# Kernel optimization log

Measured on AMD Instinct MI355X. Metric: run time of the kernel, lower is better.

Reference implementation:

```python
import jax, jax.numpy as jnp
import numpy as np
import math

DIM, H, Q_RANK, KV_RANK = 2048, 16, 768, 512
QK_STATIC, QK_ROT, V_DIM = 128, 64, 128
QK_TOTAL = QK_STATIC + QK_ROT
BS, SEQ = 2, 1024


def rmsnorm(x, scale, eps=1e-6):
    xf = x.astype(jnp.float32)
    return scale * (xf * jax.lax.rsqrt(jnp.mean(xf * xf, axis=-1, keepdims=True) + eps))


def half_rotate(x):
    h = x.shape[-1] // 2
    return jnp.concatenate([-x[..., h:], x[..., :h]], axis=-1)


def rope_tables(seq_len, dim):
    inv_freq = 1.0 / (10000.0 ** (jnp.arange(0, dim, 2, dtype=jnp.float32) / dim))
    freqs = jnp.arange(seq_len, dtype=jnp.float32)[:, None] * inv_freq[None, :]
    cos = jnp.concatenate([jnp.cos(freqs), jnp.cos(freqs)], axis=-1)  # (S, dim)
    sin = jnp.concatenate([jnp.sin(freqs), jnp.sin(freqs)], axis=-1)
    return cos, sin


def setup_inputs() -> dict:
    key = jax.random.key(0)
    ks = jax.random.split(key, 10)
    sc = lambda fan_in: 1.0 / math.sqrt(fan_in)
    x = jax.random.normal(ks[0], (BS, SEQ, DIM), dtype=jnp.float32)
    causal = jnp.where(jnp.tril(jnp.ones((SEQ, SEQ), dtype=bool)), 0.0, -1e9).astype(jnp.float32)
    mask = jnp.broadcast_to(causal[None], (BS, SEQ, SEQ))
    return {
        "x": x,
        "start_pos": 0,
        "mask": mask,
        "q_down_w": jax.random.normal(ks[1], (Q_RANK, DIM)) * sc(DIM),
        "q_down_b": jnp.zeros((Q_RANK,), jnp.float32),
        "q_norm_scale": jnp.ones((Q_RANK,), jnp.float32),
        "q_up_w": jax.random.normal(ks[2], (H * QK_TOTAL, Q_RANK)) * sc(Q_RANK),
        "q_up_b": jnp.zeros((H * QK_TOTAL,), jnp.float32),
        "kv_down_w": jax.random.normal(ks[3], (KV_RANK + QK_ROT, DIM)) * sc(DIM),
        "kv_down_b": jnp.zeros((KV_RANK + QK_ROT,), jnp.float32),
        "kv_norm_scale": jnp.ones((KV_RANK,), jnp.float32),
        "kv_up_w": jax.random.normal(ks[4], (H * (QK_STATIC + V_DIM), KV_RANK)) * sc(KV_RANK),
        "out_w": jax.random.normal(ks[5], (DIM, H * V_DIM)) * sc(H * V_DIM),
        "out_b": jnp.zeros((DIM,), jnp.float32),
    }


def reference(x, start_pos, mask, q_down_w, q_down_b, q_norm_scale, q_up_w, q_up_b,
              kv_down_w, kv_down_b, kv_norm_scale, kv_up_w, out_w, out_b):
    bs, seq_len, _ = x.shape
    # q path: down-proj -> RMSNorm -> up-proj
    q = rmsnorm(x @ q_down_w.T + q_down_b, q_norm_scale)
    q = (q @ q_up_w.T + q_up_b).reshape(bs, seq_len, H, QK_TOTAL)
    q_static, q_rot = q[..., :QK_STATIC], q[..., QK_STATIC:]
    # kv path: shared down-proj producing latent features + rotary key part
    kv = x @ kv_down_w.T + kv_down_b
    kv_feat, k_rot = kv[..., :KV_RANK], kv[..., KV_RANK:]
    # RoPE (original indexes positions 0..seq_len-1)
    cos, sin = rope_tables(seq_len, QK_ROT)
    q_rot = q_rot * cos[None, :, None, :] + half_rotate(q_rot) * sin[None, :, None, :]
    k_rot = k_rot * cos[None, :, :] + half_rotate(k_rot) * sin[None, :, :]  # (b, t, r)
    kv_normed = rmsnorm(kv_feat, kv_norm_scale)  # latent cache contents (b, t, c)
    # matrix absorption: fold kv_up key-weights into q
    w_k_abs = kv_up_w[: H * QK_STATIC, :].reshape(H, QK_STATIC, KV_RANK)
    w_v_abs = kv_up_w[-H * V_DIM :, :].reshape(H, V_DIM, KV_RANK)
    q_static_proj = jnp.einsum('bshd,hdc->bshc', q_static, w_k_abs)
    attn_scores = (jnp.einsum('bshc,btc->bsht', q_static_proj, kv_normed)
                   + jnp.einsum('bshr,btr->bsht', q_rot, k_rot)) / math.sqrt(QK_TOTAL)
    attn_scores = attn_scores + mask[:, :, None, :]
    attn_weights = jax.nn.softmax(attn_scores, axis=-1)
    # attend over latent features, then expand with absorbed value weights
    ctx_c = jnp.einsum('bsht,btc->bshc', attn_weights, kv_normed)
    ctx = jnp.einsum('bshc,hdc->bshd', ctx_c, w_v_abs)
    out = ctx.reshape(bs, seq_len, H * V_DIM) @ out_w.T + out_b
    return out
```

## Files before the change

kernel.cpp:

```cpp
#include <hip/hip_runtime.h>
#include <stdint.h>
#include <stddef.h>


typedef __attribute__((ext_vector_type(8))) short bf16x8;
typedef __attribute__((ext_vector_type(4))) float f32x4;

__device__ inline float b2f(unsigned short v){
    union { unsigned u; float f; } x; x.u = ((unsigned)v) << 16; return x.f;
}
__device__ inline unsigned short f2b(float f){
    union { float f; unsigned u; } x; x.f = f;
    unsigned r = x.u + 0x7fffu + ((x.u >> 16) & 1u);
    return (unsigned short)(r >> 16);
}

__device__ __forceinline__ void gl2lds16(const unsigned short* g, unsigned short* l){
    __builtin_amdgcn_global_load_lds(
        (__attribute__((address_space(1))) void*)const_cast<unsigned short*>(g),
        (__attribute__((address_space(3))) void*)l,
        16, 0, 0);
}

template<typename TC>
static __device__ __forceinline__ void gemm_body(
    unsigned short (*As)[4096], unsigned short (*Bs)[4096],
    const unsigned short* A, const unsigned short* B,
    const float* bias, TC* C,
    int N, int K, int lda, int ldb, int ldc,
    int m0, int n0, float alpha, int causal)
{
    const int tid = threadIdx.x, w = tid >> 6, lane = tid & 63;
    const int wm = w >> 1, wn = w & 1;

    const int srow = w * 32 + (lane >> 2);
    const int schunk = ((lane & 3) ^ ((lane >> 3) & 3)) * 8;
    const unsigned short* gA = A + (size_t)(m0 + srow) * lda + schunk;
    const unsigned short* gB = B + (size_t)(n0 + srow) * ldb + schunk;

    const int ktiles = K >> 5;
    auto stage = [&](int buf, int kt){
        const int k0 = kt << 5;
        gl2lds16(gA + k0,            &As[buf][w * 1024]);
        gl2lds16(gA + k0 + 16 * lda, &As[buf][w * 1024 + 512]);
        gl2lds16(gB + k0,            &Bs[buf][w * 1024]);
        gl2lds16(gB + k0 + 16 * ldb, &Bs[buf][w * 1024 + 512]);
    };
    stage(0, 0);
    if (ktiles > 1) stage(1, 1);

    f32x4 acc[4][4] = {};
    const int lm = lane & 15;
    const int kq = (((lane >> 4) ^ (lm >> 1)) & 3) * 8;

    int cur = 0;
    for (int kt = 0; kt < ktiles; ++kt){
        if (kt + 1 < ktiles) __builtin_amdgcn_s_waitcnt(0xF74);
        else                 __builtin_amdgcn_s_waitcnt(0xF70);
        __builtin_amdgcn_s_barrier();
        __asm__ volatile("" ::: "memory");
        if (kt + 2 < ktiles) stage(cur >= 1 ? cur - 1 : 2, kt + 2);
        bf16x8 af[4], bfr[4];
        #pragma unroll
        for (int i = 0; i < 4; ++i)
            af[i] = *(const bf16x8*)&As[cur][(wm * 64 + i * 16 + lm) * 32 + kq];
        #pragma unroll
        for (int j = 0; j < 4; ++j)
            bfr[j] = *(const bf16x8*)&Bs[cur][(wn * 64 + j * 16 + lm) * 32 + kq];
        #pragma unroll
        for (int i = 0; i < 4; ++i)
            #pragma unroll
            for (int j = 0; j < 4; ++j)
                acc[i][j] = __builtin_amdgcn_mfma_f32_16x16x32_bf16(af[i], bfr[j], acc[i][j], 0, 0, 0);
        __asm__ volatile("" ::: "memory");
        cur = (cur == 2) ? 0 : cur + 1;
    }

    #pragma unroll
    for (int i = 0; i < 4; ++i){
        const int m = m0 + wm * 64 + i * 16 + (lane >> 4) * 4;
        #pragma unroll
        for (int j = 0; j < 4; ++j){
            const int n = n0 + wn * 64 + j * 16 + lm;
            if (n < N){
                const float bb = bias ? bias[n] : 0.f;
                #pragma unroll
                for (int r = 0; r < 4; ++r){
                    float v = acc[i][j][r] * alpha + bb;
                    if ((causal & 1) && n > m + r) v = -1e9f;
                    if constexpr (sizeof(TC) == 2)
                        C[(size_t)(m + r) * ldc + n] = (TC)f2b(v);
                    else
                        C[(size_t)(m + r) * ldc + n] = (TC)v;
                }
            }
        }
    }
}

template<typename TC>
__global__ __launch_bounds__(256) void mfma_gemm_bt(
    const unsigned short* __restrict__ A, const unsigned short* __restrict__ B,
    const float* __restrict__ bias, TC* __restrict__ C,
    int M, int N, int K, int lda, int ldb, int ldc,
    int zdiv, long sA_hi, long sA_lo, long sB_hi, long sB_lo, long sC_hi, long sC_lo,
    float alpha, int causal)
{
    int z, bm, bn;
    if (causal & 4){ z = blockIdx.x; bm = blockIdx.y; bn = blockIdx.z; }
    else           { z = blockIdx.z; bm = blockIdx.y; bn = blockIdx.x; }
    int m0, n0;
    if (causal & 1){
        int i = bm;
        int mt = (int)((sqrtf(8.f * i + 1.f) - 1.f) * 0.5f);
        while ((mt + 1) * (mt + 2) / 2 <= i) ++mt;
        while (mt * (mt + 1) / 2 > i) --mt;
        n0 = (i - mt * (mt + 1) / 2) * 128;
        m0 = mt * 128;
    } else { m0 = bm * 128; n0 = bn * 128; }
    if (causal & 2) K = min(K, m0 + 128);

    __shared__ unsigned short As[3][4096];
    __shared__ unsigned short Bs[3][4096];
    const int zh = z / zdiv, zl = z % zdiv;
    A += (size_t)zh * sA_hi + (size_t)zl * sA_lo;
    B += (size_t)zh * sB_hi + (size_t)zl * sB_lo;
    C += (size_t)zh * sC_hi + (size_t)zl * sC_lo;

    gemm_body<TC>(As, Bs, A, B, bias, C, N, K, lda, ldb, ldc, m0, n0, alpha, causal);
}

__global__ __launch_bounds__(256) void mfma_gemm_vk(
    const unsigned short* __restrict__ kvuw,
    const unsigned short* __restrict__ kcat,
    unsigned short* __restrict__ vhT,
    unsigned short* __restrict__ khcat)
{
    __shared__ unsigned short As[3][4096];
    __shared__ unsigned short Bs[3][4096];
    const int p = blockIdx.x & 1, z = blockIdx.x >> 1, y = blockIdx.y;
    const int b = z >> 4, h = z & 15;
    if (p == 0){
        const unsigned short* A = kvuw + 1048576 + (size_t)h * 65536;
        const unsigned short* B = kcat + (size_t)b * 589824;
        unsigned short* C = vhT + (size_t)b * 2097152 + (size_t)h * 131072;
        gemm_body<unsigned short>(As, Bs, A, B, nullptr, C,
                                  1024, 512, 512, 576, 1024, 0, y * 128, 1.0f, 0);
    } else {
        const unsigned short* A = kcat + (size_t)b * 589824;
        const unsigned short* B = kvuw + (size_t)h * 65536;
        unsigned short* C = khcat + (size_t)b * 3145728 + (size_t)h * 196608;
        gemm_body<unsigned short>(As, Bs, A, B, nullptr, C,
                                  128, 512, 576, 512, 192, y * 128, 0, 1.0f, 0);
    }
}

__global__ __launch_bounds__(256) void flash_attn(
    const unsigned short* __restrict__ qu,
    const unsigned short* __restrict__ khcat,
    const unsigned short* __restrict__ vhT,
    unsigned short* __restrict__ ctx)
{
    const int t = blockIdx.x;
    const int r = t & 7, q = t >> 3;
    const int z = r + 8 * (q & 3);
    const int u = q >> 2;
    const int mt = (u < 8) ? (15 - 2 * u) : (2 * (u - 8));
    const int b = z >> 4, h = z & 15;
    const int m0 = mt * 64;
    const int nkt = (mt >> 1) + 1;

    __shared__ char smem[74240];
    unsigned short (*Qs)[4096] = (unsigned short (*)[4096])smem;
    unsigned short (*Ks)[8192] = (unsigned short (*)[8192])(smem + 24576);
    unsigned short* Ps = (unsigned short*)(smem + 24576);
    float* lrow = (float*)(smem + 73728);

    const unsigned short* kB = khcat + (size_t)z * 196608;
    const unsigned short* vB = vhT + (size_t)z * 131072;

    const int tid = threadIdx.x, w = tid >> 6, lane = tid & 63;
    const int wm = w >> 1, wn = w & 1;
    const int lm = lane & 15, g = lane >> 4;
    const int kq = g * 8;
    const int rs7 = lm & 7;

    if (tid < 128) lrow[tid] = 0.f;

    const int srow8 = lane >> 3;
    const int soff8 = ((lane & 7) ^ (lane >> 3)) * 8;
    const unsigned short* gQ = qu + (size_t)(b * 1024 + m0 + w * 16 + srow8) * 3072
                               + h * 192 + soff8;

    #pragma unroll
    for (int c = 0; c < 3; ++c){
        gl2lds16(gQ + c * 64,            &Qs[c][w * 1024]);
        gl2lds16(gQ + c * 64 + 8 * 3072, &Qs[c][w * 1024 + 512]);
    }

    auto stageK = [&](int buf, int kt, int c){
        const unsigned short* gK = kB + (size_t)(kt * 128 + w * 32 + srow8) * 192
                                   + c * 64 + soff8;
        gl2lds16(gK,            &Ks[buf][w * 2048]);
        gl2lds16(gK + 8 * 192,  &Ks[buf][w * 2048 + 512]);
        gl2lds16(gK + 16 * 192, &Ks[buf][w * 2048 + 1024]);
        gl2lds16(gK + 24 * 192, &Ks[buf][w * 2048 + 1536]);
    };
    stageK(2, 0, 0);

    f32x4 Oacc[2][4] = {};
    const float scl = 0.07216878364870322f;

    for (int kt = 0; kt < nkt; ++kt){
        stageK(0, kt, 1);
        stageK(1, kt, 2);
        __asm__ volatile("" ::: "memory");
        bf16x8 vfr[4][4];
        #pragma unroll
        for (int j = 0; j < 4; ++j)
            #pragma unroll
            for (int kc = 0; kc < 4; ++kc)
                vfr[j][kc] = *(const bf16x8*)(vB + (size_t)(wn * 64 + j * 16 + lm) * 1024
                                              + kt * 128 + kc * 32 + kq);
        __asm__ volatile("" ::: "memory");

        f32x4 S[2][4] = {};
        #pragma unroll
        for (int c = 0; c < 3; ++c){
            if      (c == 0) __builtin_amdgcn_s_waitcnt(0x4F78);
            else if (c == 1) __builtin_amdgcn_s_waitcnt(0x4F74);
            else             __builtin_amdgcn_s_waitcnt(0x4F70);
            __builtin_amdgcn_s_barrier();
            __asm__ volatile("" ::: "memory");
            const int bufc = (c == 0) ? 2 : (c - 1);
            bf16x8 af[2][2], bfr[4][2];
            #pragma unroll
            for (int i = 0; i < 2; ++i)
                #pragma unroll
                for (int kk = 0; kk < 2; ++kk)
                    af[i][kk] = *(const bf16x8*)&Qs[c][(wm * 32 + i * 16 + lm) * 64
                                                       + (((kk * 4 + g) ^ rs7) * 8)];
            #pragma unroll
            for (int j = 0; j < 4; ++j)
                #pragma unroll
                for (int kk = 0; kk < 2; ++kk)
                    bfr[j][kk] = *(const bf16x8*)&Ks[bufc][(wn * 64 + j * 16 + lm) * 64
                                                           + (((kk * 4 + g) ^ rs7) * 8)];
            __builtin_amdgcn_s_setprio(1);
            #pragma unroll
            for (int kk = 0; kk < 2; ++kk)
                #pragma unroll
                for (int i = 0; i < 2; ++i)
                    #pragma unroll
                    for (int j = 0; j < 4; ++j)
                        S[i][j] = __builtin_amdgcn_mfma_f32_16x16x32_bf16(af[i][kk], bfr[j][kk], S[i][j], 0, 0, 0);
            __builtin_amdgcn_s_setprio(0);
            __asm__ volatile("" ::: "memory");
        }
        __builtin_amdgcn_s_waitcnt(0xC07F);
        __builtin_amdgcn_s_barrier();
        __asm__ volatile("" ::: "memory");
        if (kt + 1 < nkt) stageK(2, kt + 1, 0);

        const bool diag = (kt == (mt >> 1));
        #pragma unroll
        for (int i = 0; i < 2; ++i){
            float rs[4] = {0.f, 0.f, 0.f, 0.f};
            #pragma unroll
            for (int j = 0; j < 4; ++j){
                const int nloc = wn * 64 + j * 16 + lm;
                #pragma unroll
                for (int r2 = 0; r2 < 4; ++r2){
                    const int mloc = wm * 32 + i * 16 + g * 4 + r2;
                    float p = __expf(S[i][j][r2] * scl);
                    if (diag && (kt * 128 + nloc) > (m0 + mloc)) p = 0.f;
                    rs[r2] += p;
                    Ps[mloc * 136 + nloc] = f2b(p);
                }
            }
            #pragma unroll
            for (int r2 = 0; r2 < 4; ++r2){
                rs[r2] += __shfl_xor(rs[r2], 1, 64);
                rs[r2] += __shfl_xor(rs[r2], 2, 64);
                rs[r2] += __shfl_xor(rs[r2], 4, 64);
                rs[r2] += __shfl_xor(rs[r2], 8, 64);
            }
            if (lm == 0){
                #pragma unroll
                for (int r2 = 0; r2 < 4; ++r2)
                    lrow[wn * 64 + wm * 32 + i * 16 + g * 4 + r2] += rs[r2];
            }
        }
        __asm__ volatile("" ::: "memory");
        __builtin_amdgcn_s_waitcnt(0xC07F);
        __builtin_amdgcn_s_barrier();
        __asm__ volatile("" ::: "memory");

        if (kt + 1 < nkt) __builtin_amdgcn_s_waitcnt(0xF74);
        else              __builtin_amdgcn_s_waitcnt(0xF70);
        #pragma unroll
        for (int kc = 0; kc < 4; ++kc){
            bf16x8 pa[2];
            #pragma unroll
            for (int i = 0; i < 2; ++i)
                pa[i] = *(const bf16x8*)&Ps[(wm * 32 + i * 16 + lm) * 136 + kc * 32 + kq];
            __builtin_amdgcn_s_setprio(1);
            #pragma unroll
            for (int i = 0; i < 2; ++i)
                #pragma unroll
                for (int j = 0; j < 4; ++j)
                    Oacc[i][j] = __builtin_amdgcn_mfma_f32_16x16x32_bf16(pa[i], vfr[j][kc], Oacc[i][j], 0, 0, 0);
            __builtin_amdgcn_s_setprio(0);
        }
        __asm__ volatile("" ::: "memory");
        __builtin_amdgcn_s_waitcnt(0xC07F);
        __builtin_amdgcn_s_barrier();
        __asm__ volatile("" ::: "memory");
    }

    unsigned short* cBase = ctx + ((size_t)(b * 1024 + m0)) * 2048 + h * 128;
    #pragma unroll
    for (int i = 0; i < 2; ++i){
        #pragma unroll
        for (int r2 = 0; r2 < 4; ++r2){
            const int row = wm * 32 + i * 16 + g * 4 + r2;
            const float inv = 1.f / (lrow[row] + lrow[64 + row]);
            #pragma unroll
            for (int j = 0; j < 4; ++j){
                const int col = wn * 64 + j * 16 + lm;
                cBase[(size_t)row * 2048 + col] = f2b(Oacc[i][j][r2] * inv);
            }
        }
    }
}

__global__ __launch_bounds__(256) void cast_all(
    const float* __restrict__ s0, unsigned short* __restrict__ d0,
    const float* __restrict__ s1, unsigned short* __restrict__ d1,
    const float* __restrict__ s2, unsigned short* __restrict__ d2,
    const float* __restrict__ s3, unsigned short* __restrict__ d3,
    const float* __restrict__ s4, unsigned short* __restrict__ d4,
    const float* __restrict__ s5, unsigned short* __restrict__ d5)
{
    long i = (long)(blockIdx.x * 256 + threadIdx.x) * 4;
    const float* s; unsigned short* d; long off;
    if      (i <  4194304L){ s = s0; d = d0; off = i; }
    else if (i <  5767168L){ s = s1; d = d1; off = i -  4194304L; }
    else if (i <  8126464L){ s = s2; d = d2; off = i -  5767168L; }
    else if (i <  9306112L){ s = s3; d = d3; off = i -  8126464L; }
    else if (i < 11403264L){ s = s4; d = d4; off = i -  9306112L; }
    else                   { s = s5; d = d5; off = i - 11403264L; }
    float4 v = *(const float4*)(s + off);
    *(ushort4*)(d + off) = make_ushort4(f2b(v.x), f2b(v.y), f2b(v.z), f2b(v.w));
}

__global__ __launch_bounds__(256) void fused_down_post(
    const unsigned short* __restrict__ p,
    const float* __restrict__ q_down_b, const float* __restrict__ kv_down_b,
    const float* __restrict__ q_norm_s, const float* __restrict__ kv_norm_s,
    unsigned short* __restrict__ qn, unsigned short* __restrict__ kcat)
{
    __shared__ float row[1344];
    __shared__ float red[4];
    const int t = blockIdx.x, tid = threadIdx.x;
    const long S = 2752512L;
    const unsigned short* b0 = p + (size_t)t * 1344;
    for (int c = tid; c < 1344; c += 256){
        float v = b2f(b0[c]) + b2f(b0[c + S]) + b2f(b0[c + 2*S]) + b2f(b0[c + 3*S]);
        v += (c < 768) ? q_down_b[c] : kv_down_b[c - 768];
        row[c] = v;
    }
    __syncthreads();
    const int lane = tid & 63, w = tid >> 6;
    float ss = 0.f;
    for (int c = tid; c < 768; c += 256){ float v = row[c]; ss += v * v; }
    #pragma unroll
    for (int o = 32; o > 0; o >>= 1) ss += __shfl_xor(ss, o, 64);
    if (lane == 0) red[w] = ss;
    __syncthreads();
    const float inv1 = rsqrtf((red[0]+red[1]+red[2]+red[3]) / 768.f + 1e-6f);
    __syncthreads();
    ss = 0.f;
    for (int c = tid; c < 512; c += 256){ float v = row[768 + c]; ss += v * v; }
    #pragma unroll
    for (int o = 32; o > 0; o >>= 1) ss += __shfl_xor(ss, o, 64);
    if (lane == 0) red[w] = ss;
    __syncthreads();
    const float inv2 = rsqrtf((red[0]+red[1]+red[2]+red[3]) / 512.f + 1e-6f);
    for (int c = tid; c < 768; c += 256)
        qn[(size_t)t * 768 + c] = f2b(q_norm_s[c] * row[c] * inv1);
    for (int c = tid; c < 512; c += 256)
        kcat[(size_t)t * 576 + c] = f2b(kv_norm_s[c] * row[768 + c] * inv2);
    if (tid < 64){
        const int d = tid, s = t & 1023;
        float x  = row[1280 + d];
        float xp = (d < 32) ? -row[1280 + d + 32] : row[1280 + d - 32];
        float ang = (float)s * powf(10000.f, -(float)(2 * (d & 31)) / 64.f);
        kcat[(size_t)t * 576 + 512 + d] = f2b(x * cosf(ang) + xp * sinf(ang));
    }
}

__global__ __launch_bounds__(256) void reduce_out(
    const unsigned short* __restrict__ p, const float* __restrict__ bias,
    float* __restrict__ out)
{
    const long S = 4194304L;
    long i = (long)(blockIdx.x * 256 + threadIdx.x) * 4;
    ushort4 a = *(const ushort4*)(p + i);
    ushort4 b = *(const ushort4*)(p + i + S);
    float4 bb = *(const float4*)(bias + (i & 2047));
    float4 r = make_float4(b2f(a.x) + b2f(b.x) + bb.x, b2f(a.y) + b2f(b.y) + bb.y,
                           b2f(a.z) + b2f(b.z) + bb.z, b2f(a.w) + b2f(b.w) + bb.w);
    *(float4*)(out + i) = r;
}

__global__ __launch_bounds__(256) void rope_q_krot(
    unsigned short* __restrict__ qu,
    const unsigned short* __restrict__ kcat,
    unsigned short* __restrict__ khcat)
{
    long idx = (long)blockIdx.x * 256 + threadIdx.x;
    if (idx < 1048576L){
        const int d   = idx & 31;
        const int h   = (idx >> 5) & 15;
        const int tok = idx >> 9;
        const int s   = tok & 1023;
        unsigned short* base = qu + (size_t)tok * 3072 + h * 192 + 128;
        float x1 = b2f(base[d]), x2 = b2f(base[d + 32]);
        float ang = (float)s * powf(10000.f, -(float)d / 32.f);
        float c = cosf(ang), sn = sinf(ang);
        base[d]      = f2b(x1 * c - x2 * sn);
        base[d + 32] = f2b(x2 * c + x1 * sn);
    } else {
        idx -= 1048576L;
        const int d   = idx & 63;
        const int h   = (idx >> 6) & 15;
        const int tok = (int)(idx >> 10);
        const int bb  = tok >> 10, s = tok & 1023;
        khcat[((size_t)(bb * 16 + h) * 1024 + s) * 192 + 128 + d] =
            kcat[(size_t)tok * 576 + 512 + d];
    }
}

extern "C" void kernel_launch(void* const* d_in, const int* in_sizes, int n_in,
                              void* d_out, int out_size, void* d_ws, size_t ws_size,
                              hipStream_t stream)
{
    const float* x         = (const float*)d_in[0];
    const float* q_down_w  = (const float*)d_in[3];
    const float* q_down_b  = (const float*)d_in[4];
    const float* q_norm_s  = (const float*)d_in[5];
    const float* q_up_w    = (const float*)d_in[6];
    const float* q_up_b    = (const float*)d_in[7];
    const float* kv_down_w = (const float*)d_in[8];
    const float* kv_down_b = (const float*)d_in[9];
    const float* kv_norm_s = (const float*)d_in[10];
    const float* kv_up_w   = (const float*)d_in[11];
    const float* out_w     = (const float*)d_in[12];
    const float* out_b     = (const float*)d_in[13];
    float* out = (float*)d_out;

    char* ws = (char*)d_ws;
    unsigned short* kvuw  = (unsigned short*)(ws + 0);
    unsigned short* outw  = (unsigned short*)(ws + 4194304);
    unsigned short* kcat  = (unsigned short*)(ws + 12582912);
    unsigned short* vhT   = (unsigned short*)(ws + 14942208);
    unsigned short* khcat = (unsigned short*)(ws + 23330816);
    unsigned short* ctx   = (unsigned short*)(ws + 35913728);
    unsigned short* qu    = (unsigned short*)(ws + 44302336);
    unsigned short* qn    = (unsigned short*)(ws + 56885248);
    unsigned short* p_qkv = (unsigned short*)(ws + 60030976);
    unsigned short* p_out = (unsigned short*)(ws + 60030976);
    unsigned short* xb    = (unsigned short*)(ws + 82051072);
    unsigned short* qkdw  = (unsigned short*)(ws + 90439680);
    unsigned short* quw   = (unsigned short*)(ws + 96206848);

    dim3 blk(256);

    cast_all<<<15232, blk, 0, stream>>>(x, xb, q_down_w, qkdw, q_up_w, quw,
                                        kv_down_w, qkdw + 1572864, kv_up_w, kvuw, out_w, outw);

    mfma_gemm_bt<unsigned short><<<dim3(11, 16, 4), blk, 0, stream>>>(
        xb, qkdw, nullptr, p_qkv, 2048, 1344, 512, 2048, 2048, 1344,
        4, 0L, 512L, 0L, 512L, 0L, 2752512L, 1.0f, 0);
    fused_down_post<<<2048, blk, 0, stream>>>(p_qkv, q_down_b, kv_down_b,
                                              q_norm_s, kv_norm_s, qn, kcat);
    mfma_gemm_bt<unsigned short><<<dim3(24, 16, 1), blk, 0, stream>>>(
        qn, quw, q_up_b, qu, 2048, 3072, 768, 768, 768, 3072,
        1, 0, 0, 0, 0, 0, 0, 1.0f, 0);
    mfma_gemm_vk<<<dim3(64, 8, 1), blk, 0, stream>>>(kvuw, kcat, vhT, khcat);
    rope_q_krot<<<12288, blk, 0, stream>>>(qu, kcat, khcat);
    flash_attn<<<dim3(512), blk, 0, stream>>>(qu, khcat, vhT, ctx);
    mfma_gemm_bt<unsigned short><<<dim3(16, 16, 2), blk, 0, stream>>>(
        ctx, outw, nullptr, p_out, 2048, 2048, 1024, 2048, 2048, 2048,
        2, 0L, 1024L, 0L, 1024L, 0L, 4194304L, 1.0f, 0);
    reduce_out<<<4096, blk, 0, stream>>>(p_out, out_b, out);
}
```

Before: 285.2 us.

## Fuse RoPE into q_up GEMM epilogue and k_rot broadcast into down-post

Removes the separate rope_q_krot kernel. The q rotary step now runs in the q_up GEMM epilogue when a wave's 64-column slice covers the rotary part of a head. The k_rot broadcast to per-head khcat rows moves into fused_down_post. It also adds an XCD-style workgroup swizzle for non-causal GEMM launches to improve L2 locality. This saves one launch and a read-modify-write pass over qu, at the cost of transcendental math inside the GEMM epilogue and extra scattered stores in the norm kernel.

```diff
diff --git a/kernel.cpp b/kernel.cpp
--- a/kernel.cpp
+++ b/kernel.cpp
@@ -76,22 +76,59 @@
         cur = (cur == 2) ? 0 : cur + 1;
     }
 
+    const bool ropeBlk = (causal & 8) && (((n0 + wn * 64) % 192) == 128);
     #pragma unroll
     for (int i = 0; i < 4; ++i){
         const int m = m0 + wm * 64 + i * 16 + (lane >> 4) * 4;
-        #pragma unroll
-        for (int j = 0; j < 4; ++j){
-            const int n = n0 + wn * 64 + j * 16 + lm;
-            if (n < N){
+        if (ropeBlk){
+            float vals[4][4];
+            #pragma unroll
+            for (int j = 0; j < 4; ++j){
+                const int n = n0 + wn * 64 + j * 16 + lm;
                 const float bb = bias ? bias[n] : 0.f;
                 #pragma unroll
+                for (int r = 0; r < 4; ++r)
+                    vals[j][r] = acc[i][j][r] * alpha + bb;
+            }
+            #pragma unroll
+            for (int jj = 0; jj < 2; ++jj){
+                const int d = jj * 16 + lm;
+                const float fr = powf(10000.f, -(float)d / 32.f);
+                #pragma unroll
                 for (int r = 0; r < 4; ++r){
-                    float v = acc[i][j][r] * alpha + bb;
-                    if ((causal & 1) && n > m + r) v = -1e9f;
+                    const float ang = (float)((m + r) & 1023) * fr;
+                    const float cs = cosf(ang), sn = sinf(ang);
+                    const float x1 = vals[jj][r], x2 = vals[jj + 2][r];
+                    vals[jj][r]     = x1 * cs - x2 * sn;
+                    vals[jj + 2][r] = x2 * cs + x1 * sn;
+                }
+            }
+            #pragma unroll
+            for (int j = 0; j < 4; ++j){
+                const int n = n0 + wn * 64 + j * 16 + lm;
+                #pragma unroll
+                for (int r = 0; r < 4; ++r){
                     if constexpr (sizeof(TC) == 2)
-                        C[(size_t)(m + r) * ldc + n] = (TC)f2b(v);
+                        C[(size_t)(m + r) * ldc + n] = (TC)f2b(vals[j][r]);
                     else
-                        C[(size_t)(m + r) * ldc + n] = (TC)v;
+                        C[(size_t)(m + r) * ldc + n] = (TC)vals[j][r];
+                }
+            }
+        } else {
+            #pragma unroll
+            for (int j = 0; j < 4; ++j){
+                const int n = n0 + wn * 64 + j * 16 + lm;
+                if (n < N){
+                    const float bb = bias ? bias[n] : 0.f;
+                    #pragma unroll
+                    for (int r = 0; r < 4; ++r){
+                        float v = acc[i][j][r] * alpha + bb;
+                        if ((causal & 1) && n > m + r) v = -1e9f;
+                        if constexpr (sizeof(TC) == 2)
+                            C[(size_t)(m + r) * ldc + n] = (TC)f2b(v);
+                        else
+                            C[(size_t)(m + r) * ldc + n] = (TC)v;
+                    }
                 }
             }
         }
@@ -109,6 +146,15 @@
     int z, bm, bn;
     if (causal & 4){ z = blockIdx.x; bm = blockIdx.y; bn = blockIdx.z; }
     else           { z = blockIdx.z; bm = blockIdx.y; bn = blockIdx.x; }
+    if (!(causal & 5)){
+        const int gx = (int)gridDim.x;
+        const int nwg = gx * (int)gridDim.y;
+        if ((nwg & 7) == 0){
+            const int lid = bn + gx * bm;
+            const int swz = (lid & 7) * (nwg >> 3) + (lid >> 3);
+            bm = swz / gx; bn = swz % gx;
+        }
+    }
     int m0, n0;
     if (causal & 1){
         int i = bm;
@@ -358,7 +404,8 @@
     const unsigned short* __restrict__ p,
     const float* __restrict__ q_down_b, const float* __restrict__ kv_down_b,
     const float* __restrict__ q_norm_s, const float* __restrict__ kv_norm_s,
-    unsigned short* __restrict__ qn, unsigned short* __restrict__ kcat)
+    unsigned short* __restrict__ qn, unsigned short* __restrict__ kcat,
+    unsigned short* __restrict__ khcat)
 {
     __shared__ float row[1344];
     __shared__ float red[4];
@@ -396,7 +443,12 @@
         float x  = row[1280 + d];
         float xp = (d < 32) ? -row[1280 + d + 32] : row[1280 + d - 32];
         float ang = (float)s * powf(10000.f, -(float)(2 * (d & 31)) / 64.f);
-        kcat[(size_t)t * 576 + 512 + d] = f2b(x * cosf(ang) + xp * sinf(ang));
+        const unsigned short kv = f2b(x * cosf(ang) + xp * sinf(ang));
+        kcat[(size_t)t * 576 + 512 + d] = kv;
+        const size_t base = ((size_t)((t >> 10) * 16) * 1024 + s) * 192 + 128 + d;
+        #pragma unroll
+        for (int h = 0; h < 16; ++h)
+            khcat[base + (size_t)h * 196608] = kv;
     }
 }
 
@@ -412,34 +464,6 @@
     float4 r = make_float4(b2f(a.x) + b2f(b.x) + bb.x, b2f(a.y) + b2f(b.y) + bb.y,
                            b2f(a.z) + b2f(b.z) + bb.z, b2f(a.w) + b2f(b.w) + bb.w);
     *(float4*)(out + i) = r;
-}
-
-__global__ __launch_bounds__(256) void rope_q_krot(
-    unsigned short* __restrict__ qu,
-    const unsigned short* __restrict__ kcat,
-    unsigned short* __restrict__ khcat)
-{
-    long idx = (long)blockIdx.x * 256 + threadIdx.x;
-    if (idx < 1048576L){
-        const int d   = idx & 31;
-        const int h   = (idx >> 5) & 15;
-        const int tok = idx >> 9;
-        const int s   = tok & 1023;
-        unsigned short* base = qu + (size_t)tok * 3072 + h * 192 + 128;
-        float x1 = b2f(base[d]), x2 = b2f(base[d + 32]);
-        float ang = (float)s * powf(10000.f, -(float)d / 32.f);
-        float c = cosf(ang), sn = sinf(ang);
-        base[d]      = f2b(x1 * c - x2 * sn);
-        base[d + 32] = f2b(x2 * c + x1 * sn);
-    } else {
-        idx -= 1048576L;
-        const int d   = idx & 63;
-        const int h   = (idx >> 6) & 15;
-        const int tok = (int)(idx >> 10);
-        const int bb  = tok >> 10, s = tok & 1023;
-        khcat[((size_t)(bb * 16 + h) * 1024 + s) * 192 + 128 + d] =
-            kcat[(size_t)tok * 576 + 512 + d];
-    }
 }
 
 extern "C" void kernel_launch(void* const* d_in, const int* in_sizes, int n_in,
@@ -484,12 +508,11 @@
         xb, qkdw, nullptr, p_qkv, 2048, 1344, 512, 2048, 2048, 1344,
         4, 0L, 512L, 0L, 512L, 0L, 2752512L, 1.0f, 0);
     fused_down_post<<<2048, blk, 0, stream>>>(p_qkv, q_down_b, kv_down_b,
-                                              q_norm_s, kv_norm_s, qn, kcat);
+                                              q_norm_s, kv_norm_s, qn, kcat, khcat);
     mfma_gemm_bt<unsigned short><<<dim3(24, 16, 1), blk, 0, stream>>>(
         qn, quw, q_up_b, qu, 2048, 3072, 768, 768, 768, 3072,
-        1, 0, 0, 0, 0, 0, 0, 1.0f, 0);
+        1, 0, 0, 0, 0, 0, 0, 1.0f, 8);
     mfma_gemm_vk<<<dim3(64, 8, 1), blk, 0, stream>>>(kvuw, kcat, vhT, khcat);
-    rope_q_krot<<<12288, blk, 0, stream>>>(qu, kcat, khcat);
     flash_attn<<<dim3(512), blk, 0, stream>>>(qu, khcat, vhT, ctx);
     mfma_gemm_bt<unsigned short><<<dim3(16, 16, 2), blk, 0, stream>>>(
         ctx, outw, nullptr, p_out, 2048, 2048, 1024, 2048, 2048, 2048,
```

Result: slower. 323.7 us (+13.5%).
